# Kernel optimization log

Measured on AMD Instinct MI355X. Metric: run time of the kernel, lower is better.

## Reference

```python
import jax, jax.numpy as jnp
import numpy as np

B, T, S, M = 1024, 256, 16, 4  # groups, timesteps, num_states, num_measurements


def setup_inputs() -> dict:
    key = jax.random.key(0)
    ks = jax.random.split(key, 6)
    inp = jax.random.normal(ks[0], (B, T, M), dtype=jnp.float32)
    # Stable transition matrix (spectral radius < 1 so the 256-step scan doesn't blow up)
    F = (0.95 * jnp.eye(S) + 0.05 * jax.random.normal(ks[1], (S, S)) / np.sqrt(S)).astype(jnp.float32)
    H = (jax.random.normal(ks[2], (M, S)) / np.sqrt(S)).astype(jnp.float32)
    q = 0.1 * jax.random.normal(ks[3], (S, S))
    Q = (q @ q.T / S + 1e-3 * jnp.eye(S)).astype(jnp.float32)  # PSD process noise
    r = 0.1 * jax.random.normal(ks[4], (M, M))
    R = (r @ r.T / M + 1e-3 * jnp.eye(M)).astype(jnp.float32)  # PSD measurement noise
    initial_state = jax.random.normal(ks[5], (S,), dtype=jnp.float32)
    initial_std_dev = jnp.ones((S,), dtype=jnp.float32)
    return {"input": inp, "F": F, "H": H, "Q": Q, "R": R,
            "initial_state": initial_state, "initial_std_dev": initial_std_dev}


def _kf_forward(input, F, H, Q, R, initial_state, initial_std_dev):
    bs, nt, nm = input.shape
    ns = F.shape[0]
    eyeS = jnp.eye(ns, dtype=input.dtype)

    # default_initializer: mean = initial_state, cov = diag(std_dev)^2, expanded over batch
    x0 = jnp.broadcast_to(initial_state[None, :, None], (bs, ns, 1))
    P0 = jnp.broadcast_to(jnp.diag(initial_std_dev ** 2)[None], (bs, ns, ns))

    def kf_predict(x, P):
        x = jnp.einsum('ij,bjo->bio', F, x)                     # F x
        P = jnp.einsum('ij,bjk,lk->bil', F, P, F) + Q           # F P F^T + Q
        return x, P

    def kf_update(obs_t, x, P):
        resid = obs_t[:, :, None] - jnp.einsum('ms,bso->bmo', H, x)      # [B,M,1]
        Smat = jnp.einsum('ms,bst,nt->bmn', H, P, H) + R                 # [B,M,M]
        # K = P H^T S^{-1}; since S is symmetric, K^T = solve(S, H P)
        K = jnp.linalg.solve(Smat, jnp.einsum('ms,bst->bmt', H, P)).swapaxes(-1, -2)  # [B,S,M]
        x_new = x + K @ resid
        # Joseph-stabilized covariance update: (I-KH) P (I-KH)^T + K R K^T
        ImKH = eyeS - jnp.einsum('bsm,mt->bst', K, H)
        P_new = ImKH @ P @ ImKH.swapaxes(-1, -2) + jnp.einsum('bsm,mn,btn->bst', K, R, K)
        return x_new, P_new

    # t = -1: predict from the initializer, emitted as the prediction for time 0
    x, P = kf_predict(x0, P0)
    first = x

    obs_seq = jnp.swapaxes(input[:, :-1, :], 0, 1)  # [T-1, B, M], time-major

    def step(carry, obs_t):
        x, P = carry
        x, P = kf_update(obs_t, x, P)
        x, P = kf_predict(x, P)
        return (x, P), x

    _, ys = jax.lax.scan(step, (x, P), obs_seq)      # ys: [T-1, B, S, 1]
    means = jnp.concatenate([first[None], ys], 0)     # [T, B, S, 1]
    # out = H @ means, reshaped to [B, T, M] (matches view(T,B,M).transpose(0,1))
    out = jnp.einsum('ms,tbso->btm', H, means)
    return out


def reference(input, F, H, Q, R, initial_state, initial_std_dev):
    return _kf_forward(input, F, H, Q, R, initial_state, initial_std_dev)
```

## Files before the change

### kernel.cpp

```cpp
#include <hip/hip_runtime.h>

#define NT 256
#define NSTEP 255
#define FREEZE_T 40

__device__ __forceinline__ float dot4(float4 a, float4 b) {
    return a.x*b.x + a.y*b.y + a.z*b.z + a.w*b.w;
}

__device__ __forceinline__ void gather16_issue(float zr, float (&zk)[16]) {
    asm volatile (
         "ds_swizzle_b32 %0,  %16 offset:16\n\t"
         "ds_swizzle_b32 %1,  %16 offset:48\n\t"
         "ds_swizzle_b32 %2,  %16 offset:80\n\t"
         "ds_swizzle_b32 %3,  %16 offset:112\n\t"
         "ds_swizzle_b32 %4,  %16 offset:144\n\t"
         "ds_swizzle_b32 %5,  %16 offset:176\n\t"
         "ds_swizzle_b32 %6,  %16 offset:208\n\t"
         "ds_swizzle_b32 %7,  %16 offset:240\n\t"
         "ds_swizzle_b32 %8,  %16 offset:272\n\t"
         "ds_swizzle_b32 %9,  %16 offset:304\n\t"
         "ds_swizzle_b32 %10, %16 offset:336\n\t"
         "ds_swizzle_b32 %11, %16 offset:368\n\t"
         "ds_swizzle_b32 %12, %16 offset:400\n\t"
         "ds_swizzle_b32 %13, %16 offset:432\n\t"
         "ds_swizzle_b32 %14, %16 offset:464\n\t"
         "ds_swizzle_b32 %15, %16 offset:496"
         : "=&v"(zk[0]),  "=&v"(zk[1]),  "=&v"(zk[2]),  "=&v"(zk[3]),
           "=&v"(zk[4]),  "=&v"(zk[5]),  "=&v"(zk[6]),  "=&v"(zk[7]),
           "=&v"(zk[8]),  "=&v"(zk[9]),  "=&v"(zk[10]), "=&v"(zk[11]),
           "=&v"(zk[12]), "=&v"(zk[13]), "=&v"(zk[14]), "=&v"(zk[15])
         : "v"(zr));
}

__device__ __forceinline__ void gather16(float zr, float (&zk)[16]) {
    asm ("ds_swizzle_b32 %0,  %16 offset:16\n\t"
         "ds_swizzle_b32 %1,  %16 offset:48\n\t"
         "ds_swizzle_b32 %2,  %16 offset:80\n\t"
         "ds_swizzle_b32 %3,  %16 offset:112\n\t"
         "ds_swizzle_b32 %4,  %16 offset:144\n\t"
         "ds_swizzle_b32 %5,  %16 offset:176\n\t"
         "ds_swizzle_b32 %6,  %16 offset:208\n\t"
         "ds_swizzle_b32 %7,  %16 offset:240\n\t"
         "ds_swizzle_b32 %8,  %16 offset:272\n\t"
         "ds_swizzle_b32 %9,  %16 offset:304\n\t"
         "ds_swizzle_b32 %10, %16 offset:336\n\t"
         "ds_swizzle_b32 %11, %16 offset:368\n\t"
         "ds_swizzle_b32 %12, %16 offset:400\n\t"
         "ds_swizzle_b32 %13, %16 offset:432\n\t"
         "ds_swizzle_b32 %14, %16 offset:464\n\t"
         "ds_swizzle_b32 %15, %16 offset:496\n\t"
         "s_waitcnt lgkmcnt(0)"
         : "=&v"(zk[0]),  "=&v"(zk[1]),  "=&v"(zk[2]),  "=&v"(zk[3]),
           "=&v"(zk[4]),  "=&v"(zk[5]),  "=&v"(zk[6]),  "=&v"(zk[7]),
           "=&v"(zk[8]),  "=&v"(zk[9]),  "=&v"(zk[10]), "=&v"(zk[11]),
           "=&v"(zk[12]), "=&v"(zk[13]), "=&v"(zk[14]), "=&v"(zk[15])
         : "v"(zr));
}

__device__ __forceinline__ void xgather12(const float (&pc)[4],
                                          float (&b16)[4], float (&b32)[4], float (&b48)[4],
                                          int a16, int a32, int a48)
{
    asm volatile (
         "ds_bpermute_b32 %0,  %16, %12\n\t"
         "ds_bpermute_b32 %1,  %16, %13\n\t"
         "ds_bpermute_b32 %2,  %16, %14\n\t"
         "ds_bpermute_b32 %3,  %16, %15\n\t"
         "ds_bpermute_b32 %4,  %17, %12\n\t"
         "ds_bpermute_b32 %5,  %17, %13\n\t"
         "ds_bpermute_b32 %6,  %17, %14\n\t"
         "ds_bpermute_b32 %7,  %17, %15\n\t"
         "ds_bpermute_b32 %8,  %18, %12\n\t"
         "ds_bpermute_b32 %9,  %18, %13\n\t"
         "ds_bpermute_b32 %10, %18, %14\n\t"
         "ds_bpermute_b32 %11, %18, %15\n\t"
         "s_waitcnt lgkmcnt(0)"
         : "=&v"(b16[0]), "=&v"(b16[1]), "=&v"(b16[2]), "=&v"(b16[3]),
           "=&v"(b32[0]), "=&v"(b32[1]), "=&v"(b32[2]), "=&v"(b32[3]),
           "=&v"(b48[0]), "=&v"(b48[1]), "=&v"(b48[2]), "=&v"(b48[3])
         : "v"(pc[0]), "v"(pc[1]), "v"(pc[2]), "v"(pc[3]),
           "v"(a16), "v"(a32), "v"(a48));
}

__device__ __forceinline__ void vmatA2(const float (&vin1)[16], const float (&vin2)[16],
                                       float (&vout1)[16], float (&vout2)[16],
                                       const float4* sA4) {
#pragma unroll
    for (int c = 0; c < 16; ++c) { vout1[c] = 0.f; vout2[c] = 0.f; }
#pragma unroll
    for (int k = 0; k < 16; ++k) {
#pragma unroll
        for (int f = 0; f < 4; ++f) {
            float4 av = sA4[k*5 + f];
            vout1[4*f+0] = fmaf(vin1[k], av.x, vout1[4*f+0]);
            vout1[4*f+1] = fmaf(vin1[k], av.y, vout1[4*f+1]);
            vout1[4*f+2] = fmaf(vin1[k], av.z, vout1[4*f+2]);
            vout1[4*f+3] = fmaf(vin1[k], av.w, vout1[4*f+3]);
            vout2[4*f+0] = fmaf(vin2[k], av.x, vout2[4*f+0]);
            vout2[4*f+1] = fmaf(vin2[k], av.y, vout2[4*f+1]);
            vout2[4*f+2] = fmaf(vin2[k], av.z, vout2[4*f+2]);
            vout2[4*f+3] = fmaf(vin2[k], av.w, vout2[4*f+3]);
        }
    }
}

__global__ __launch_bounds__(64) void kf_block_kernel(
    const float* __restrict__ obs, const float* __restrict__ Fg,
    const float* __restrict__ Hg,  const float* __restrict__ Qg,
    const float* __restrict__ Rg,  const float* __restrict__ x0g,
    const float* __restrict__ sdg, float* __restrict__ out)
{
    __shared__ float4 sF4[80];
    __shared__ float4 sA4[80];
    __shared__ float4 sAP4[80];
    __shared__ float4 sHP4[16];
    __shared__ float4 sV4[16];
    __shared__ float4 sB4[16];
    __shared__ float4 sS4[4];
    __shared__ float  sZ[16];
    __shared__ float4 sObs4[1024];
    __shared__ float4 sOut4[1024];

    float* sF  = (float*)sF4;
    float* sA  = (float*)sA4;
    float* sAP = (float*)sAP4;
    float* sHP = (float*)sHP4;
    float* sV  = (float*)sV4;
    float* sB  = (float*)sB4;
    float* sS  = (float*)sS4;
    float* sOut = (float*)sOut4;

    const int tid = threadIdx.x;
    const int q  = tid >> 4;
    const int j  = tid & 15;
    const int bi = tid >> 2;
    const int bm = tid & 3;
    const int a16 = (tid ^ 16) << 2, a32 = (tid ^ 32) << 2, a48 = (tid ^ 48) << 2;

    const float4* Fg4 = (const float4*)Fg;
    const float4* Hg4 = (const float4*)Hg;
    const float4* Rg4 = (const float4*)Rg;
    const float4* obs4g = (const float4*)obs;

    for (int u = tid; u < 1024; u += 64)
        sObs4[u] = obs4g[(blockIdx.x * 4 + (u >> 8)) * NT + (u & 255)];
    for (int u = tid; u < 256; u += 64) sF[(u >> 4) * 20 + (u & 15)] = Fg[u];

    float wF[4][4][4], wH[4][4];
#pragma unroll
    for (int r2 = 0; r2 < 4; ++r2)
#pragma unroll
        for (int X = 0; X < 4; ++X)
#pragma unroll
            for (int r = 0; r < 4; ++r)
                wF[r2][X][r] = Fg[(q + 4*r2)*16 + ((q ^ X) + 4*r)];
#pragma unroll
    for (int X = 0; X < 4; ++X)
#pragma unroll
        for (int r = 0; r < 4; ++r)
            wH[X][r] = Hg[q*16 + ((q ^ X) + 4*r)];

    float4 zFbi[4], zHn[4], zHrow4[4];
#pragma unroll
    for (int f = 0; f < 4; ++f) {
        zFbi[f]   = Fg4[bi*4 + f];
        zHn[f]    = Hg4[bm*4 + f];
        zHrow4[f] = Hg4[(j & 3)*4 + f];
    }
    float hr[16] = {zHrow4[0].x,zHrow4[0].y,zHrow4[0].z,zHrow4[0].w,
                    zHrow4[1].x,zHrow4[1].y,zHrow4[1].z,zHrow4[1].w,
                    zHrow4[2].x,zHrow4[2].y,zHrow4[2].z,zHrow4[2].w,
                    zHrow4[3].x,zHrow4[3].y,zHrow4[3].z,zHrow4[3].w};
    float zQ[4];
#pragma unroll
    for (int r = 0; r < 4; ++r) zQ[r] = Qg[(q + 4*r)*16 + j];
    float  zRs = Rg[tid & 15];
    float4 zR4[4];
#pragma unroll
    for (int m = 0; m < 4; ++m) zR4[m] = Rg4[m];
    float4 zHcjv = make_float4(Hg[j], Hg[16 + j], Hg[32 + j], Hg[48 + j]);
    float4 zFijv = make_float4(Fg[q*16 + j],      Fg[(q+4)*16 + j],
                               Fg[(q+8)*16 + j],  Fg[(q+12)*16 + j]);

    float pc[4];
    {
        float wFj_[4][4], sd2p[4][4];
#pragma unroll
        for (int X = 0; X < 4; ++X)
#pragma unroll
            for (int r = 0; r < 4; ++r) {
                int k = (q ^ X) + 4*r;
                wFj_[X][r] = Fg[j*16 + k];
                float s = sdg[k];
                sd2p[X][r] = s*s;
            }
#pragma unroll
        for (int r2 = 0; r2 < 4; ++r2) {
            float acc = zQ[r2];
#pragma unroll
            for (int X = 0; X < 4; ++X)
#pragma unroll
                for (int r = 0; r < 4; ++r)
                    acc = fmaf(wF[r2][X][r] * sd2p[X][r], wFj_[X][r], acc);
            pc[r2] = acc;
        }
    }
    __syncthreads();

    if (tid < 16) {
        float acc = 0.f;
#pragma unroll
        for (int f = 0; f < 4; ++f) {
            float4 fr = ((float4*)(sF + tid*20))[f];
            float4 xv = ((const float4*)x0g)[f];
            acc += dot4(fr, xv);
        }
        sZ[tid] = acc;
    }
    __syncthreads();
    float zr = sZ[j];

#pragma unroll 1
    for (int t = 0; t < FREEZE_T; ++t) {
        float zk[16];
        float4 oo = sObs4[q*256 + t];
        gather16_issue(zr, zk);
        float b16[4], b32[4], b48[4];
        xgather12(pc, b16, b32, b48, a16, a32, a48);
        float tf[4], hp;
#pragma unroll
        for (int r2 = 0; r2 < 4; ++r2) {
            float acc = 0.f;
#pragma unroll
            for (int r = 0; r < 4; ++r) {
                acc = fmaf(wF[r2][0][r], pc[r],
                      fmaf(wF[r2][1][r], b16[r],
                      fmaf(wF[r2][2][r], b32[r],
                      fmaf(wF[r2][3][r], b48[r], acc))));
            }
            tf[r2] = acc;
        }
        {
            float acc = 0.f;
#pragma unroll
            for (int r = 0; r < 4; ++r) {
                acc = fmaf(wH[0][r], pc[r],
                      fmaf(wH[1][r], b16[r],
                      fmaf(wH[2][r], b32[r],
                      fmaf(wH[3][r], b48[r], acc))));
            }
            hp = acc;
        }
        sHP[q*16 + j] = hp;
        __syncthreads();

        {
            float acc = 0.f;
#pragma unroll
            for (int f = 0; f < 4; ++f) acc += dot4(zFbi[f], sHP4[bm*4 + f]);
            sV[bi*4 + bm] = acc;
        }
        if (tid < 16) {
            float acc = zRs;
#pragma unroll
            for (int f = 0; f < 4; ++f) acc += dot4(sHP4[(tid >> 2)*4 + f], zHn[f]);
            sS[tid] = acc;
        }
        __syncthreads();

        {
            int ra = (bm == 0) ? 1 : 0;
            int rb = (bm <= 1) ? 2 : 1;
            int rc = (bm <= 2) ? 3 : 2;
            float4 a = sS4[ra], b = sS4[rb], c = sS4[rc], sm = sS4[bm];
            float M0 = a.y*(b.z*c.w - b.w*c.z) - a.z*(b.y*c.w - b.w*c.y) + a.w*(b.y*c.z - b.z*c.y);
            float M1 = a.x*(b.z*c.w - b.w*c.z) - a.z*(b.x*c.w - b.w*c.x) + a.w*(b.x*c.z - b.z*c.x);
            float M2 = a.x*(b.y*c.w - b.w*c.y) - a.y*(b.x*c.w - b.w*c.x) + a.w*(b.x*c.y - b.y*c.x);
            float M3 = a.x*(b.y*c.z - b.z*c.y) - a.y*(b.x*c.z - b.z*c.x) + a.z*(b.x*c.y - b.y*c.x);
            float sg = (bm & 1) ? -1.f : 1.f;
            float c0 = sg*M0, c1 = -sg*M1, c2 = sg*M2, c3 = -sg*M3;
            float det = sm.x*c0 + sm.y*c1 + sm.z*c2 + sm.w*c3;
            float4 vv = sV4[bi];
            sB[tid] = (vv.x*c0 + vv.y*c1 + vv.z*c2 + vv.w*c3) / det;
        }
        __syncthreads();

        float4 bq[4], rbtv;
        {
            float4 hpcv = make_float4(sHP[j], sHP[16 + j], sHP[32 + j], sHP[48 + j]);
            float4 bj = sB4[j];
#pragma unroll
            for (int r = 0; r < 4; ++r) {
                int i = q + 4*r;
                bq[r] = sB4[i];
                float av = ((const float*)&zFijv)[r] - dot4(bq[r], zHcjv);
                float ap = tf[r] - dot4(bq[r], hpcv);
                sA[i*20 + j]  = av;
                sAP[i*20 + j] = ap;
            }
            rbtv = make_float4(dot4(zR4[0], bj), dot4(zR4[1], bj),
                               dot4(zR4[2], bj), dot4(zR4[3], bj));
        }
        __syncthreads();

        float4 zA[4];
#pragma unroll
        for (int f = 0; f < 4; ++f) zA[f] = sA4[j*5 + f];
#pragma unroll
        for (int r = 0; r < 4; ++r) {
            int i = q + 4*r;
            float acc = zQ[r] + dot4(bq[r], rbtv);
#pragma unroll
            for (int f = 0; f < 4; ++f) acc += dot4(sAP4[i*5 + f], zA[f]);
            pc[r] = acc;
        }
        {
            float arr[16] = {zA[0].x,zA[0].y,zA[0].z,zA[0].w,
                             zA[1].x,zA[1].y,zA[1].z,zA[1].w,
                             zA[2].x,zA[2].y,zA[2].z,zA[2].w,
                             zA[3].x,zA[3].y,zA[3].z,zA[3].w};
            float4 bb = sB4[j];
            float o0 = 0.f, o1 = 0.f, zn0 = 0.f, zn1 = dot4(bb, oo);
#pragma unroll
            for (int k = 0; k < 8; ++k) {
                o0  = fmaf(hr[k],      zk[k],     o0);
                zn0 = fmaf(arr[k],     zk[k],     zn0);
            }
#pragma unroll
            for (int k = 8; k < 16; ++k) {
                o1  = fmaf(hr[k],      zk[k],     o1);
                zn1 = fmaf(arr[k],     zk[k],     zn1);
            }
            if (j < 4) sOut[(q*256 + t)*4 + j] = o0 + o1;
            zr = zn0 + zn1;
        }
    }

    float arF[16];
    float4 bbF;
    {
        float4 a0 = sA4[j*5 + 0], a1 = sA4[j*5 + 1], a2 = sA4[j*5 + 2], a3 = sA4[j*5 + 3];
        arF[0]=a0.x; arF[1]=a0.y; arF[2]=a0.z; arF[3]=a0.w;
        arF[4]=a1.x; arF[5]=a1.y; arF[6]=a1.z; arF[7]=a1.w;
        arF[8]=a2.x; arF[9]=a2.y; arF[10]=a2.z; arF[11]=a2.w;
        arF[12]=a3.x; arF[13]=a3.y; arF[14]=a3.z; arF[15]=a3.w;
        bbF = sB4[j];
    }

    {
        float hA1[16], hA2[16], hA3[16], A2r[16], A3r[16], A4r[16];
        vmatA2(hr,  arF, hA1, A2r, sA4);
        vmatA2(hA1, A2r, hA2, A3r, sA4);
        vmatA2(hA2, A3r, hA3, A4r, sA4);
        float4 hB  = make_float4(0,0,0,0), hB1 = make_float4(0,0,0,0),
               hB2 = make_float4(0,0,0,0), ab1 = make_float4(0,0,0,0),
               ab2 = make_float4(0,0,0,0), ab3 = make_float4(0,0,0,0);
#pragma unroll
        for (int k = 0; k < 16; ++k) {
            float4 bv = sB4[k];
            hB.x  = fmaf(hr[k],  bv.x, hB.x);  hB.y  = fmaf(hr[k],  bv.y, hB.y);
            hB.z  = fmaf(hr[k],  bv.z, hB.z);  hB.w  = fmaf(hr[k],  bv.w, hB.w);
            hB1.x = fmaf(hA1[k], bv.x, hB1.x); hB1.y = fmaf(hA1[k], bv.y, hB1.y);
            hB1.z = fmaf(hA1[k], bv.z, hB1.z); hB1.w = fmaf(hA1[k], bv.w, hB1.w);
            hB2.x = fmaf(hA2[k], bv.x, hB2.x); hB2.y = fmaf(hA2[k], bv.y, hB2.y);
            hB2.z = fmaf(hA2[k], bv.z, hB2.z); hB2.w = fmaf(hA2[k], bv.w, hB2.w);
            ab1.x = fmaf(arF[k], bv.x, ab1.x); ab1.y = fmaf(arF[k], bv.y, ab1.y);
            ab1.z = fmaf(arF[k], bv.z, ab1.z); ab1.w = fmaf(arF[k], bv.w, ab1.w);
            ab2.x = fmaf(A2r[k], bv.x, ab2.x); ab2.y = fmaf(A2r[k], bv.y, ab2.y);
            ab2.z = fmaf(A2r[k], bv.z, ab2.z); ab2.w = fmaf(A2r[k], bv.w, ab2.w);
            ab3.x = fmaf(A3r[k], bv.x, ab3.x); ab3.y = fmaf(A3r[k], bv.y, ab3.y);
            ab3.z = fmaf(A3r[k], bv.z, ab3.z); ab3.w = fmaf(A3r[k], bv.w, ab3.w);
        }

        int tt = FREEZE_T;
#pragma unroll 1
        for (; tt + 3 < NSTEP; tt += 4) {
            float4 u0 = sObs4[q*256 + tt];
            float4 u1 = sObs4[q*256 + tt + 1];
            float4 u2 = sObs4[q*256 + tt + 2];
            float4 u3 = sObs4[q*256 + tt + 3];
            float zk[16];
            gather16(zr, zk);
            float o0a = 0.f,             o0b = 0.f;
            float o1a = dot4(hB, u0),    o1b = 0.f;
            float o2a = dot4(hB1, u0),   o2b = dot4(hB, u1);
            float o3a = dot4(hB2, u0),   o3b = dot4(hB1, u1) + dot4(hB, u2);
            float za  = dot4(ab3, u0) + dot4(ab2, u1),
                  zb  = dot4(ab1, u2) + dot4(bbF, u3);
#pragma unroll
            for (int k = 0; k < 8; ++k) {
                o0a = fmaf(hr[k],  zk[k], o0a);
                o1a = fmaf(hA1[k], zk[k], o1a);
                o2a = fmaf(hA2[k], zk[k], o2a);
                o3a = fmaf(hA3[k], zk[k], o3a);
                za  = fmaf(A4r[k], zk[k], za);
            }
#pragma unroll
            for (int k = 8; k < 16; ++k) {
                o0b = fmaf(hr[k],  zk[k], o0b);
                o1b = fmaf(hA1[k], zk[k], o1b);
                o2b = fmaf(hA2[k], zk[k], o2b);
                o3b = fmaf(hA3[k], zk[k], o3b);
                zb  = fmaf(A4r[k], zk[k], zb);
            }
            if (j < 4) {
                sOut[(q*256 + tt    )*4 + j] = o0a + o0b;
                sOut[(q*256 + tt + 1)*4 + j] = o1a + o1b;
                sOut[(q*256 + tt + 2)*4 + j] = o2a + o2b;
                sOut[(q*256 + tt + 3)*4 + j] = o3a + o3b;
            }
            zr = za + zb;
        }
#pragma unroll 1
        for (; tt < NSTEP; ++tt) {
            float4 oo = sObs4[q*256 + tt];
            float zk[16];
            gather16(zr, zk);
            float o0 = 0.f, o1 = 0.f, zn0 = 0.f, zn1 = dot4(bbF, oo);
#pragma unroll
            for (int k = 0; k < 8; ++k) {
                o0  = fmaf(hr[k],  zk[k], o0);
                zn0 = fmaf(arF[k], zk[k], zn0);
            }
#pragma unroll
            for (int k = 8; k < 16; ++k) {
                o1  = fmaf(hr[k],  zk[k], o1);
                zn1 = fmaf(arF[k], zk[k], zn1);
            }
            if (j < 4) sOut[(q*256 + tt)*4 + j] = o0 + o1;
            zr = zn0 + zn1;
        }
    }
    {
        float zk[16];
        gather16(zr, zk);
        float o0 = 0.f, o1 = 0.f;
#pragma unroll
        for (int k = 0; k < 8; ++k)  o0 = fmaf(hr[k], zk[k], o0);
#pragma unroll
        for (int k = 8; k < 16; ++k) o1 = fmaf(hr[k], zk[k], o1);
        if (j < 4) sOut[(q*256 + 255)*4 + j] = o0 + o1;
    }
    __syncthreads();
    float4* out4 = (float4*)out;
    for (int u = tid; u < 1024; u += 64)
        out4[(blockIdx.x * 4 + (u >> 8)) * NT + (u & 255)] = sOut4[u];
}

extern "C" void kernel_launch(void* const* d_in, const int* in_sizes, int n_in,
                              void* d_out, int out_size, void* d_ws, size_t ws_size,
                              hipStream_t stream) {
    const float* obs = (const float*)d_in[0];
    const float* F   = (const float*)d_in[1];
    const float* H   = (const float*)d_in[2];
    const float* Q   = (const float*)d_in[3];
    const float* R   = (const float*)d_in[4];
    const float* x0  = (const float*)d_in[5];
    const float* sd  = (const float*)d_in[6];
    float* out = (float*)d_out;

    hipLaunchKernelGGL(kf_block_kernel, dim3(256), dim3(64), 0, stream,
                       obs, F, H, Q, R, x0, sd, out);
}
```

Before: 146.3 us.

## Software-pipeline cross-lane gathers across Kalman and frozen-gain recurrence steps

Splits the ds_swizzle/ds_bpermute gathers into issue and wait halves so they are in flight while other arithmetic runs. In the covariance phase, the mean update for step t is deferred to the next iteration and the P-column gathers are issued at the end of each step. In the frozen-gain tail, the next state gather is issued right after the new state is computed, overlapping it with the output dot products via double-buffered zk registers. This shortens the serial latency chain per step, but needs more registers and depends on hand-placed lgkmcnt waits and sched barriers being correct.

```diff
diff --git a/kernel.cpp b/kernel.cpp
--- a/kernel.cpp
+++ b/kernel.cpp
@@ -58,9 +58,8 @@
          : "v"(zr));
 }
 
-__device__ __forceinline__ void xgather12(const float (&pc)[4],
-                                          float (&b16)[4], float (&b32)[4], float (&b48)[4],
-                                          int a16, int a32, int a48)
+__device__ __forceinline__ void xgather12_issue(const float (&pc)[4],
+    float (&b16)[4], float (&b32)[4], float (&b48)[4], int a16, int a32, int a48)
 {
     asm volatile (
          "ds_bpermute_b32 %0,  %16, %12\n\t"
@@ -74,8 +73,7 @@
          "ds_bpermute_b32 %8,  %18, %12\n\t"
          "ds_bpermute_b32 %9,  %18, %13\n\t"
          "ds_bpermute_b32 %10, %18, %14\n\t"
-         "ds_bpermute_b32 %11, %18, %15\n\t"
-         "s_waitcnt lgkmcnt(0)"
+         "ds_bpermute_b32 %11, %18, %15"
          : "=&v"(b16[0]), "=&v"(b16[1]), "=&v"(b16[2]), "=&v"(b16[3]),
            "=&v"(b32[0]), "=&v"(b32[1]), "=&v"(b32[2]), "=&v"(b32[3]),
            "=&v"(b48[0]), "=&v"(b48[1]), "=&v"(b48[2]), "=&v"(b48[3])
@@ -221,13 +219,46 @@
     __syncthreads();
     float zr = sZ[j];
 
+    float b16[4], b32[4], b48[4], zk[16];
+    float4 zAp[4] = {};
+    float4 bjp = make_float4(0,0,0,0);
+    xgather12_issue(pc, b16, b32, b48, a16, a32, a48);
+    gather16_issue(zr, zk);
+
 #pragma unroll 1
     for (int t = 0; t < FREEZE_T; ++t) {
-        float zk[16];
-        float4 oo = sObs4[q*256 + t];
-        gather16_issue(zr, zk);
-        float b16[4], b32[4], b48[4];
-        xgather12(pc, b16, b32, b48, a16, a32, a48);
+        asm volatile("s_waitcnt lgkmcnt(12)"
+            : "+v"(zk[0]), "+v"(zk[1]), "+v"(zk[2]),  "+v"(zk[3]),
+              "+v"(zk[4]), "+v"(zk[5]), "+v"(zk[6]),  "+v"(zk[7]),
+              "+v"(zk[8]), "+v"(zk[9]), "+v"(zk[10]), "+v"(zk[11]),
+              "+v"(zk[12]),"+v"(zk[13]),"+v"(zk[14]), "+v"(zk[15]));
+        __builtin_amdgcn_sched_barrier(0);
+        if (t > 0) {
+            float arr[16] = {zAp[0].x,zAp[0].y,zAp[0].z,zAp[0].w,
+                             zAp[1].x,zAp[1].y,zAp[1].z,zAp[1].w,
+                             zAp[2].x,zAp[2].y,zAp[2].z,zAp[2].w,
+                             zAp[3].x,zAp[3].y,zAp[3].z,zAp[3].w};
+            float4 oo = sObs4[q*256 + (t-1)];
+            float o0 = 0.f, o1 = 0.f, zn0 = 0.f, zn1 = 0.f;
+#pragma unroll
+            for (int k = 0; k < 8; ++k) {
+                o0  = fmaf(hr[k],  zk[k], o0);
+                zn0 = fmaf(arr[k], zk[k], zn0);
+            }
+#pragma unroll
+            for (int k = 8; k < 16; ++k) {
+                o1  = fmaf(hr[k],  zk[k], o1);
+                zn1 = fmaf(arr[k], zk[k], zn1);
+            }
+            zn1 += dot4(bjp, oo);
+            if (j < 4) sOut[(q*256 + (t-1))*4 + j] = o0 + o1;
+            zr = zn0 + zn1;
+        }
+        asm volatile("s_waitcnt lgkmcnt(0)"
+            : "+v"(b16[0]), "+v"(b16[1]), "+v"(b16[2]), "+v"(b16[3]),
+              "+v"(b32[0]), "+v"(b32[1]), "+v"(b32[2]), "+v"(b32[3]),
+              "+v"(b48[0]), "+v"(b48[1]), "+v"(b48[2]), "+v"(b48[3]));
+        __builtin_amdgcn_sched_barrier(0);
         float tf[4], hp;
 #pragma unroll
         for (int r2 = 0; r2 < 4; ++r2) {
@@ -253,6 +284,7 @@
             hp = acc;
         }
         sHP[q*16 + j] = hp;
+        gather16_issue(zr, zk);
         __syncthreads();
 
         {
@@ -289,7 +321,7 @@
         float4 bq[4], rbtv;
         {
             float4 hpcv = make_float4(sHP[j], sHP[16 + j], sHP[32 + j], sHP[48 + j]);
-            float4 bj = sB4[j];
+            bjp = sB4[j];
 #pragma unroll
             for (int r = 0; r < 4; ++r) {
                 int i = q + 4*r;
@@ -299,54 +331,59 @@
                 sA[i*20 + j]  = av;
                 sAP[i*20 + j] = ap;
             }
-            rbtv = make_float4(dot4(zR4[0], bj), dot4(zR4[1], bj),
-                               dot4(zR4[2], bj), dot4(zR4[3], bj));
+            rbtv = make_float4(dot4(zR4[0], bjp), dot4(zR4[1], bjp),
+                               dot4(zR4[2], bjp), dot4(zR4[3], bjp));
         }
         __syncthreads();
 
-        float4 zA[4];
-#pragma unroll
-        for (int f = 0; f < 4; ++f) zA[f] = sA4[j*5 + f];
+#pragma unroll
+        for (int f = 0; f < 4; ++f) zAp[f] = sA4[j*5 + f];
 #pragma unroll
         for (int r = 0; r < 4; ++r) {
             int i = q + 4*r;
             float acc = zQ[r] + dot4(bq[r], rbtv);
 #pragma unroll
-            for (int f = 0; f < 4; ++f) acc += dot4(sAP4[i*5 + f], zA[f]);
+            for (int f = 0; f < 4; ++f) acc += dot4(sAP4[i*5 + f], zAp[f]);
             pc[r] = acc;
         }
-        {
-            float arr[16] = {zA[0].x,zA[0].y,zA[0].z,zA[0].w,
-                             zA[1].x,zA[1].y,zA[1].z,zA[1].w,
-                             zA[2].x,zA[2].y,zA[2].z,zA[2].w,
-                             zA[3].x,zA[3].y,zA[3].z,zA[3].w};
-            float4 bb = sB4[j];
-            float o0 = 0.f, o1 = 0.f, zn0 = 0.f, zn1 = dot4(bb, oo);
-#pragma unroll
-            for (int k = 0; k < 8; ++k) {
-                o0  = fmaf(hr[k],      zk[k],     o0);
-                zn0 = fmaf(arr[k],     zk[k],     zn0);
-            }
-#pragma unroll
-            for (int k = 8; k < 16; ++k) {
-                o1  = fmaf(hr[k],      zk[k],     o1);
-                zn1 = fmaf(arr[k],     zk[k],     zn1);
-            }
-            if (j < 4) sOut[(q*256 + t)*4 + j] = o0 + o1;
-            zr = zn0 + zn1;
-        }
-    }
+        xgather12_issue(pc, b16, b32, b48, a16, a32, a48);
+    }
+
+    asm volatile("s_waitcnt lgkmcnt(0)"
+        : "+v"(b16[0]), "+v"(b16[1]), "+v"(b16[2]), "+v"(b16[3]),
+          "+v"(b32[0]), "+v"(b32[1]), "+v"(b32[2]), "+v"(b32[3]),
+          "+v"(b48[0]), "+v"(b48[1]), "+v"(b48[2]), "+v"(b48[3]),
+          "+v"(zk[0]),  "+v"(zk[1]),  "+v"(zk[2]),  "+v"(zk[3]),
+          "+v"(zk[4]),  "+v"(zk[5]),  "+v"(zk[6]),  "+v"(zk[7]),
+          "+v"(zk[8]),  "+v"(zk[9]),  "+v"(zk[10]), "+v"(zk[11]),
+          "+v"(zk[12]), "+v"(zk[13]), "+v"(zk[14]), "+v"(zk[15]));
+    __builtin_amdgcn_sched_barrier(0);
 
     float arF[16];
-    float4 bbF;
     {
-        float4 a0 = sA4[j*5 + 0], a1 = sA4[j*5 + 1], a2 = sA4[j*5 + 2], a3 = sA4[j*5 + 3];
-        arF[0]=a0.x; arF[1]=a0.y; arF[2]=a0.z; arF[3]=a0.w;
-        arF[4]=a1.x; arF[5]=a1.y; arF[6]=a1.z; arF[7]=a1.w;
-        arF[8]=a2.x; arF[9]=a2.y; arF[10]=a2.z; arF[11]=a2.w;
-        arF[12]=a3.x; arF[13]=a3.y; arF[14]=a3.z; arF[15]=a3.w;
-        bbF = sB4[j];
-    }
+        float arr[16] = {zAp[0].x,zAp[0].y,zAp[0].z,zAp[0].w,
+                         zAp[1].x,zAp[1].y,zAp[1].z,zAp[1].w,
+                         zAp[2].x,zAp[2].y,zAp[2].z,zAp[2].w,
+                         zAp[3].x,zAp[3].y,zAp[3].z,zAp[3].w};
+        float4 oo = sObs4[q*256 + (FREEZE_T-1)];
+        float o0 = 0.f, o1 = 0.f, zn0 = 0.f, zn1 = 0.f;
+#pragma unroll
+        for (int k = 0; k < 8; ++k) {
+            o0  = fmaf(hr[k],  zk[k], o0);
+            zn0 = fmaf(arr[k], zk[k], zn0);
+        }
+#pragma unroll
+        for (int k = 8; k < 16; ++k) {
+            o1  = fmaf(hr[k],  zk[k], o1);
+            zn1 = fmaf(arr[k], zk[k], zn1);
+        }
+        zn1 += dot4(bjp, oo);
+        if (j < 4) sOut[(q*256 + (FREEZE_T-1))*4 + j] = o0 + o1;
+        zr = zn0 + zn1;
+#pragma unroll
+        for (int k = 0; k < 16; ++k) arF[k] = arr[k];
+    }
+    float4 bbF = bjp;
 
     {
         float hA1[16], hA2[16], hA3[16], A2r[16], A3r[16], A4r[16];
@@ -373,36 +410,43 @@
             ab3.z = fmaf(A3r[k], bv.z, ab3.z); ab3.w = fmaf(A3r[k], bv.w, ab3.w);
         }
 
-        int tt = FREEZE_T;
-#pragma unroll 1
-        for (; tt + 3 < NSTEP; tt += 4) {
-            float4 u0 = sObs4[q*256 + tt];
-            float4 u1 = sObs4[q*256 + tt + 1];
-            float4 u2 = sObs4[q*256 + tt + 2];
-            float4 u3 = sObs4[q*256 + tt + 3];
-            float zk[16];
-            gather16(zr, zk);
+        float zkA[16], zkB[16];
+        float4 u0 = sObs4[q*256 + FREEZE_T],     u1 = sObs4[q*256 + FREEZE_T + 1],
+               u2 = sObs4[q*256 + FREEZE_T + 2], u3 = sObs4[q*256 + FREEZE_T + 3];
+        gather16_issue(zr, zkA);
+
+        auto tail4 = [&](int tt, float (&ZIN)[16], float (&ZOUT)[16]) {
+            asm volatile("s_waitcnt lgkmcnt(0)"
+                : "+v"(ZIN[0]), "+v"(ZIN[1]), "+v"(ZIN[2]),  "+v"(ZIN[3]),
+                  "+v"(ZIN[4]), "+v"(ZIN[5]), "+v"(ZIN[6]),  "+v"(ZIN[7]),
+                  "+v"(ZIN[8]), "+v"(ZIN[9]), "+v"(ZIN[10]), "+v"(ZIN[11]),
+                  "+v"(ZIN[12]),"+v"(ZIN[13]),"+v"(ZIN[14]), "+v"(ZIN[15]));
+            __builtin_amdgcn_sched_barrier(0);
+            float za = dot4(ab3, u0) + dot4(ab2, u1);
+            float zb = dot4(ab1, u2) + dot4(bbF, u3);
+#pragma unroll
+            for (int k = 0; k < 8; ++k)  za = fmaf(A4r[k], ZIN[k], za);
+#pragma unroll
+            for (int k = 8; k < 16; ++k) zb = fmaf(A4r[k], ZIN[k], zb);
+            zr = za + zb;
+            gather16_issue(zr, ZOUT);
             float o0a = 0.f,             o0b = 0.f;
             float o1a = dot4(hB, u0),    o1b = 0.f;
             float o2a = dot4(hB1, u0),   o2b = dot4(hB, u1);
             float o3a = dot4(hB2, u0),   o3b = dot4(hB1, u1) + dot4(hB, u2);
-            float za  = dot4(ab3, u0) + dot4(ab2, u1),
-                  zb  = dot4(ab1, u2) + dot4(bbF, u3);
 #pragma unroll
             for (int k = 0; k < 8; ++k) {
-                o0a = fmaf(hr[k],  zk[k], o0a);
-                o1a = fmaf(hA1[k], zk[k], o1a);
-                o2a = fmaf(hA2[k], zk[k], o2a);
-                o3a = fmaf(hA3[k], zk[k], o3a);
-                za  = fmaf(A4r[k], zk[k], za);
+                o0a = fmaf(hr[k],  ZIN[k], o0a);
+                o1a = fmaf(hA1[k], ZIN[k], o1a);
+                o2a = fmaf(hA2[k], ZIN[k], o2a);
+                o3a = fmaf(hA3[k], ZIN[k], o3a);
             }
 #pragma unroll
             for (int k = 8; k < 16; ++k) {
-                o0b = fmaf(hr[k],  zk[k], o0b);
-                o1b = fmaf(hA1[k], zk[k], o1b);
-                o2b = fmaf(hA2[k], zk[k], o2b);
-                o3b = fmaf(hA3[k], zk[k], o3b);
-                zb  = fmaf(A4r[k], zk[k], zb);
+                o0b = fmaf(hr[k],  ZIN[k], o0b);
+                o1b = fmaf(hA1[k], ZIN[k], o1b);
+                o2b = fmaf(hA2[k], ZIN[k], o2b);
+                o3b = fmaf(hA3[k], ZIN[k], o3b);
             }
             if (j < 4) {
                 sOut[(q*256 + tt    )*4 + j] = o0a + o0b;
@@ -410,36 +454,53 @@
                 sOut[(q*256 + tt + 2)*4 + j] = o2a + o2b;
                 sOut[(q*256 + tt + 3)*4 + j] = o3a + o3b;
             }
-            zr = za + zb;
-        }
+            u0 = sObs4[q*256 + tt + 4]; u1 = sObs4[q*256 + tt + 5];
+            u2 = sObs4[q*256 + tt + 6]; u3 = sObs4[q*256 + tt + 7];
+        };
+
+        int tt = FREEZE_T;
+#pragma unroll 1
+        for (; tt + 7 < NSTEP; tt += 8) {
+            tail4(tt,     zkA, zkB);
+            tail4(tt + 4, zkB, zkA);
+        }
+        tail4(tt, zkA, zkB);
+        tt += 4;
+        asm volatile("s_waitcnt lgkmcnt(0)"
+            : "+v"(zkB[0]), "+v"(zkB[1]), "+v"(zkB[2]),  "+v"(zkB[3]),
+              "+v"(zkB[4]), "+v"(zkB[5]), "+v"(zkB[6]),  "+v"(zkB[7]),
+              "+v"(zkB[8]), "+v"(zkB[9]), "+v"(zkB[10]), "+v"(zkB[11]),
+              "+v"(zkB[12]),"+v"(zkB[13]),"+v"(zkB[14]), "+v"(zkB[15]));
+        __builtin_amdgcn_sched_barrier(0);
+
 #pragma unroll 1
         for (; tt < NSTEP; ++tt) {
             float4 oo = sObs4[q*256 + tt];
-            float zk[16];
-            gather16(zr, zk);
+            float zs[16];
+            gather16(zr, zs);
             float o0 = 0.f, o1 = 0.f, zn0 = 0.f, zn1 = dot4(bbF, oo);
 #pragma unroll
             for (int k = 0; k < 8; ++k) {
-                o0  = fmaf(hr[k],  zk[k], o0);
-                zn0 = fmaf(arF[k], zk[k], zn0);
+                o0  = fmaf(hr[k],  zs[k], o0);
+                zn0 = fmaf(arF[k], zs[k], zn0);
             }
 #pragma unroll
             for (int k = 8; k < 16; ++k) {
-                o1  = fmaf(hr[k],  zk[k], o1);
-                zn1 = fmaf(arF[k], zk[k], zn1);
+                o1  = fmaf(hr[k],  zs[k], o1);
+                zn1 = fmaf(arF[k], zs[k], zn1);
             }
             if (j < 4) sOut[(q*256 + tt)*4 + j] = o0 + o1;
             zr = zn0 + zn1;
         }
     }
     {
-        float zk[16];
-        gather16(zr, zk);
+        float zs[16];
+        gather16(zr, zs);
         float o0 = 0.f, o1 = 0.f;
 #pragma unroll
-        for (int k = 0; k < 8; ++k)  o0 = fmaf(hr[k], zk[k], o0);
-#pragma unroll
-        for (int k = 8; k < 16; ++k) o1 = fmaf(hr[k], zk[k], o1);
+        for (int k = 0; k < 8; ++k)  o0 = fmaf(hr[k], zs[k], o0);
+#pragma unroll
+        for (int k = 8; k < 16; ++k) o1 = fmaf(hr[k], zs[k], o1);
         if (j < 4) sOut[(q*256 + 255)*4 + j] = o0 + o1;
     }
     __syncthreads();
```

New measurement: 153.4 us. 4.9% more time.
